# Optimization experiments

Measured on AMD Instinct MI355X. Metric: run time of the kernel, lower is better.

## Reference

```python
import jax, jax.numpy as jnp
import numpy as np
import math

D = 128
RATIO = 0.8
BN_EPS = 1e-5
N_NODES = 40000
N_EDGES = 640000
Y_SIZE = 8


def _prelu(x, a):
    return jnp.where(x > 0, x, a * x)


def setup_inputs() -> dict:
    key = jax.random.key(0)
    ks = jax.random.split(key, 16)
    inv = lambda n: 1.0 / np.sqrt(n)
    return {
        "x": jax.random.normal(ks[0], (N_NODES, 1), jnp.float32),
        "edge_index": jax.random.randint(ks[1], (2, N_EDGES), 0, N_NODES, jnp.int32),
        "W1": jax.random.normal(ks[2], (1, D), jnp.float32),
        "V1": jax.random.normal(ks[3], (1, D), jnp.float32),
        "Ws": jax.random.normal(ks[4], (9, D, D), jnp.float32) * inv(D),
        "Vs": jax.random.normal(ks[5], (9, D, D), jnp.float32) * inv(D),
        "conv_b": jax.random.normal(ks[6], (10, D), jnp.float32) * 0.01,
        "bn_gamma": 1.0 + 0.1 * jax.random.normal(ks[7], (10, D), jnp.float32),
        "bn_beta": 0.1 * jax.random.normal(ks[8], (10, D), jnp.float32),
        "bn_mean": jnp.zeros((10, D), jnp.float32),
        "bn_var": jnp.ones((10, D), jnp.float32),
        "pool_p": jax.random.normal(ks[9], (10, D), jnp.float32),
        "prelu_a": 0.25 * jnp.ones((1,), jnp.float32),
        "lin1_w": jax.random.normal(ks[10], (2560, 1280), jnp.float32) * inv(2560),
        "lin1_b": jax.random.normal(ks[11], (1280,), jnp.float32) * 0.01,
        "lin2_w": jax.random.normal(ks[12], (1280, Y_SIZE), jnp.float32) * inv(1280),
        "lin2_b": jax.random.normal(ks[13], (Y_SIZE,), jnp.float32) * 0.01,
    }


def reference(x, edge_index, W1, V1, Ws, Vs, conv_b, bn_gamma, bn_beta, bn_mean,
              bn_var, pool_p, prelu_a, lin1_w, lin1_b, lin2_w, lin2_b):
    # Single graph (batch all zeros). Edge array stays fixed size with a validity mask.
    src, dst = edge_index[0], edge_index[1]
    emask = jnp.ones(src.shape, dtype=bool)
    n = x.shape[0]
    h = x
    reads = []
    for i in range(10):
        W = W1 if i == 0 else Ws[i - 1]
        V = V1 if i == 0 else Vs[i - 1]
        # ---- ARMAConv (num_stacks=1, num_layers=1): relu(L_hat (h W) + h V + b)
        ew = emask.astype(h.dtype)
        deg = jax.ops.segment_sum(ew, dst, num_segments=n)
        dinv = jnp.where(deg > 0, 1.0 / jnp.sqrt(deg), 0.0)
        norm = dinv[dst] * dinv[src] * ew                      # [E]
        hw = h @ W                                             # [n, D]
        agg = jax.ops.segment_sum(hw[src] * norm[:, None], dst, num_segments=n)
        h = jax.nn.relu(agg + h @ V + conv_b[i])
        # ---- BatchNorm1d (eval mode, running stats)
        h = (h - bn_mean[i]) * (bn_gamma[i] / jnp.sqrt(bn_var[i] + BN_EPS)) + bn_beta[i]
        # ---- shared PReLU
        h = _prelu(h, prelu_a)
        # ---- TopKPooling(ratio=0.8): score = tanh(h.p/||p||), keep ceil(0.8n)
        p = pool_p[i]
        score = jnp.tanh(h @ p / jnp.linalg.norm(p))
        k = math.ceil(RATIO * n)
        topv, idx = jax.lax.top_k(score, k)
        h = h[idx] * topv[:, None]                             # [k, D]
        remap = jnp.full((n,), -1, jnp.int32).at[idx].set(jnp.arange(k, dtype=jnp.int32))
        ns, nd = remap[src], remap[dst]
        emask = emask & (ns >= 0) & (nd >= 0)
        src = jnp.where(emask, ns, 0)
        dst = jnp.where(emask, nd, 0)
        n = k
        # ---- global max + mean pool (single graph)
        reads.append(jnp.concatenate([h.max(axis=0), h.mean(axis=0)]))
    r = jnp.concatenate(reads)[None, :]                        # [1, 2560]
    z = _prelu(r @ lin1_w + lin1_b, prelu_a)                   # dropout = identity (eval)
    z = _prelu(z @ lin2_w + lin2_b, prelu_a)
    z = z - z.min(axis=1, keepdims=True)
    z = z / z.max(axis=1, keepdims=True)
    z = z / z.sum(axis=1, keepdims=True)
    return z
```

## Files before the change

kernel.cpp:

```cpp
#include <hip/hip_runtime.h>
#include <hip/hip_bf16.h>

#define NEDGE 640000
#define NMAX  40000
#define SB    40
#define PRB   256
#define EBLK  512
#define FB    1280
#define LIN1B 64
#define GRB   16
#define HTS   20
#define TKB   32
#define GHN   5632
#define GBMAX 2048

__device__ inline unsigned orderKey(float s) {
    unsigned b = __float_as_uint(s);
    return (b & 0x80000000u) ? ~b : (b | 0x80000000u);
}

__device__ inline void histAdd(int* sh, int bin, bool act, int nbits) {
    unsigned long long mm = __ballot(act);
    for (int b = 0; b < nbits; b++) {
        unsigned long long bal = __ballot(act && ((bin >> b) & 1));
        mm &= ((bin >> b) & 1) ? bal : ~bal;
    }
    if (act) {
        int lane = threadIdx.x & 63;
        int leader = __ffsll(mm) - 1;
        if (lane == leader) atomicAdd(&sh[bin], __popcll(mm));
    }
}

__device__ inline void gridbar(int* ctr, int target) {
    __syncthreads();
    if (threadIdx.x == 0) {
        __threadfence();
        __hip_atomic_fetch_add(ctr, 1, __ATOMIC_RELEASE, __HIP_MEMORY_SCOPE_AGENT);
        while (__hip_atomic_load(ctr, __ATOMIC_ACQUIRE, __HIP_MEMORY_SCOPE_AGENT) < target)
            __builtin_amdgcn_s_sleep(1);
        __threadfence();
    }
    __syncthreads();
}

__device__ inline int waveScanIncl(int v) {
    int lane = threadIdx.x & 63;
    #pragma unroll
    for (int off = 1; off < 64; off <<= 1) {
        int o = __shfl_up(v, off);
        if (lane >= off) v += o;
    }
    return v;
}

__device__ inline void selScan2048(const int* gh, int rem, int* outD, int* outR, int* outCnt) {
    __shared__ int wtot[16];
    __shared__ int s_T;
    int t = threadIdx.x, lane = t & 63, wid = t >> 6;
    int a0 = gh[2*t], a1 = gh[2*t+1];
    int s  = a0 + a1;
    int ws = waveScanIncl(s);
    if (lane == 63) wtot[wid] = ws;
    __syncthreads();
    if (t < 16) {
        int v = wtot[t];
        #pragma unroll
        for (int off = 1; off < 16; off <<= 1) { int o = __shfl_up(v, off); if (lane >= off) v += o; }
        wtot[t] = v;
        if (t == 15) s_T = v;
    }
    __syncthreads();
    int base = (wid > 0) ? wtot[wid-1] : 0;
    int inclPair = base + ws;
    int P1 = inclPair - a1;
    int P0 = P1 - a0;
    int Q = s_T - rem;
    if (a0 > 0 && P0 <= Q && Q < P0 + a0) { *outD = 2*t;   *outR = a0 - (Q - P0); *outCnt = a0; }
    if (a1 > 0 && P1 <= Q && Q < P1 + a1) { *outD = 2*t+1; *outR = a1 - (Q - P1); *outCnt = a1; }
    __syncthreads();
}

__device__ inline void selScan1024(const int* gh, int rem, int* outD, int* outR, int* outCnt) {
    __shared__ int wtot[16];
    __shared__ int s_T;
    int t = threadIdx.x, lane = t & 63, wid = t >> 6;
    int a0 = gh[t];
    int ws = waveScanIncl(a0);
    if (lane == 63) wtot[wid] = ws;
    __syncthreads();
    if (t < 16) {
        int v = wtot[t];
        #pragma unroll
        for (int off = 1; off < 16; off <<= 1) { int o = __shfl_up(v, off); if (lane >= off) v += o; }
        wtot[t] = v;
        if (t == 15) s_T = v;
    }
    __syncthreads();
    int base = (wid > 0) ? wtot[wid-1] : 0;
    int P0 = base + ws - a0;
    int Q = s_T - rem;
    if (a0 > 0 && P0 <= Q && Q < P0 + a0) { *outD = t; *outR = a0 - (Q - P0); *outCnt = a0; }
    __syncthreads();
}

__device__ inline void prefixSel256(int* lh, const int* gh, int rem, int* outD, int* outR) {
    int t = threadIdx.x;
    if (t < 256) lh[t] = gh[t];
    __syncthreads();
    for (int off = 1; off < 256; off <<= 1) {
        int v = 0;
        if (t < 256) v = lh[t] + ((t >= off) ? lh[t-off] : 0);
        __syncthreads();
        if (t < 256) lh[t] = v;
        __syncthreads();
    }
    if (t < 256) {
        int P = lh[t], Pp = (t == 0) ? 0 : lh[t-1];
        if (P >= rem && Pp < rem) { *outD = t; *outR = rem - Pp; }
    }
    __syncthreads();
}

__device__ inline void poolReduceC(const float* __restrict__ scr, float* __restrict__ rbuf,
                                   int gbP, int L, int ch) {
    int t = threadIdx.x;
    bool isMax = ch < 128;
    float acc = isMax ? -3.402823e38f : 0.f;
    for (int r = t; r < gbP; r += 256) {
        float v = scr[(size_t)r*256 + ch];
        acc = isMax ? fmaxf(acc, v) : (acc + v);
    }
    __shared__ float red[256];
    red[t] = acc; __syncthreads();
    for (int st = 128; st > 0; st >>= 1) {
        if (t < st) red[t] = isMax ? fmaxf(red[t], red[t+st]) : (red[t] + red[t+st]);
        __syncthreads();
    }
    if (t == 0) rbuf[L*256 + ch] = red[0];
}

__device__ const float c_invk[10] = {
    1.0f/32000.0f, 1.0f/25600.0f, 1.0f/20480.0f, 1.0f/16384.0f, 1.0f/13108.0f,
    1.0f/10487.0f, 1.0f/8390.0f,  1.0f/6712.0f,  1.0f/5370.0f,  1.0f/4296.0f };

__global__ void k_init(const int* __restrict__ eidx, int* __restrict__ esrc,
                       int* __restrict__ edst, int* __restrict__ erank,
                       const float* __restrict__ poolp,
                       float* __restrict__ rbuf, float* __restrict__ pnorm,
                       int* __restrict__ ecnt, int* __restrict__ degA,
                       int* __restrict__ tkc) {
    int b = blockIdx.x, t = threadIdx.x;
    if (b < 10) {
        rbuf[b*256 + t] = (t < 128) ? -3.402823e38f : 0.0f;
        __shared__ float red[256];
        float v = 0.0f;
        if (t < 128) { float pv = poolp[b*128 + t]; v = pv*pv; }
        red[t] = v; __syncthreads();
        for (int s = 128; s > 0; s >>= 1) { if (t < s) red[t] += red[t+s]; __syncthreads(); }
        if (t == 0) pnorm[b] = sqrtf(red[0]);
    }
    if (b == 10 && t < 16) ecnt[t] = (t == 0) ? NEDGE : 0;
    if (b == 11 && t < 64) tkc[t] = 0;
    int e = b*256 + t;
    if (e < NEDGE) {
        int d = eidx[NEDGE + e];
        esrc[e] = eidx[e]; edst[e] = d;
        erank[e] = atomicAdd(&degA[d], 1);
    }
}

__global__ __launch_bounds__(256) void k_presum(const int* __restrict__ deg,
                                                int* __restrict__ lbsum,
                                                int n, int chunk) {
    int b = blockIdx.x, t = threadIdx.x;
    __shared__ int red[256];
    int start = b*chunk, end = min(start + chunk, n);
    int s = 0;
    for (int i = start + t; i < end; i += 256) s += deg[i];
    red[t] = s; __syncthreads();
    for (int st = 128; st > 0; st >>= 1) { if (t < st) red[t] += red[t+st]; __syncthreads(); }
    if (t == 0) lbsum[b] = red[0];
}

__global__ void k_scan(const int* __restrict__ deg,
                       int* __restrict__ offs, float* __restrict__ dinv,
                       int* __restrict__ ghist, int* __restrict__ selbuf,
                       const int* __restrict__ lbsum,
                       const float* __restrict__ scr, float* __restrict__ rbuf,
                       int n, int chunk, int gbP, int prevL) {
    int b = blockIdx.x, t = threadIdx.x, lane = t & 63, wid = t >> 6;
    if (b >= SB) {
        if (gbP > 0) poolReduceC(scr, rbuf, gbP, prevL, b - SB);
        return;
    }
    __shared__ int s_excl;
    __shared__ int wsum[4];
    __shared__ int s_carry;
    __shared__ int s_sums[SB];
    if (b == 0) {
        for (int jj = t; jj < GHN; jj += 256) ghist[jj] = 0;
        if (t == 0) { selbuf[2] = 0; selbuf[5] = 0; }
    }
    if (t < SB) s_sums[t] = lbsum[t];
    __syncthreads();
    if (t == 0) {
        int excl = 0;
        for (int p = 0; p < b; p++) excl += s_sums[p];
        s_excl = excl;
    }
    __syncthreads();
    if (t == 0) s_carry = s_excl;
    __syncthreads();
    int start = b*chunk, end = min(start + chunk, n);
    for (int base = start; base < end; base += 256) {
        int i = base + t;
        int d = (i < end) ? deg[i] : 0;
        int incl = d;
        for (int off = 1; off < 64; off <<= 1) {
            int o = __shfl_up(incl, off);
            if (lane >= off) incl += o;
        }
        if (lane == 63) wsum[wid] = incl;
        __syncthreads();
        if (t == 0) { int c = s_carry; for (int w = 0; w < 4; w++) { int tmp = wsum[w]; wsum[w] = c; c += tmp; } s_carry = c; }
        __syncthreads();
        int p = wsum[wid] + incl - d;
        if (i < end) {
            offs[i] = p;
            dinv[i] = (d > 0) ? 1.0f/sqrtf((float)d) : 0.0f;
        }
        __syncthreads();
    }
}

__global__ __launch_bounds__(128) void k_fill(const int* __restrict__ esrc, const int* __restrict__ edst,
                                              const int* __restrict__ erank, const int* __restrict__ offs,
                                              int* __restrict__ csr, const int* __restrict__ ecnt) {
    int ec = *ecnt;
    for (int e = blockIdx.x*128 + threadIdx.x; e < ec; e += FB*128)
        csr[offs[edst[e]] + erank[e]] = esrc[e];
}

__global__ __launch_bounds__(128) void k_gather0(
    const float* __restrict__ x, const float* __restrict__ W1, const float* __restrict__ V1,
    const float* __restrict__ convb,
    const float* __restrict__ bng, const float* __restrict__ bnb,
    const float* __restrict__ bnm, const float* __restrict__ bnv,
    const float* __restrict__ poolp, const float* __restrict__ pnorm,
    const float* __restrict__ prelua,
    const int* __restrict__ offs, const int* __restrict__ deg, const float* __restrict__ dinv,
    const int* __restrict__ csr,
    float* __restrict__ AGG, float* __restrict__ score, unsigned* __restrict__ keys) {
    int v = blockIdx.x, j = threadIdx.x;
    __shared__ float red[128];
    int off = offs[v], dg = deg[v];
    float accs = 0.0f;
    for (int c = j; c < dg; c += 128) { int s = csr[off + c]; accs += x[s]*dinv[s]; }
    red[j] = accs; __syncthreads();
    for (int st = 64; st > 0; st >>= 1) { if (j < st) red[j] += red[j+st]; __syncthreads(); }
    float aggs = red[0] * dinv[v];
    __syncthreads();
    float h2 = aggs*W1[j] + x[v]*V1[j] + convb[j];
    h2 = fmaxf(h2, 0.0f);
    float scale = bng[j] / sqrtf(bnv[j] + 1e-5f);
    h2 = (h2 - bnm[j])*scale + bnb[j];
    float a = prelua[0];
    h2 = (h2 > 0.0f) ? h2 : a*h2;
    AGG[v*128 + j] = h2;
    red[j] = h2 * poolp[j]; __syncthreads();
    for (int st = 64; st > 0; st >>= 1) { if (j < st) red[j] += red[j+st]; __syncthreads(); }
    if (j == 0) {
        float sc = tanhf(red[0] / pnorm[0]);
        score[v] = sc;
        keys[v]  = orderKey(sc);
    }
}

__global__ __launch_bounds__(128) void k_gather(
    const float* __restrict__ HW, float* __restrict__ AGG,
    const int* __restrict__ offs, const int* __restrict__ deg, const float* __restrict__ dinv,
    const int* __restrict__ csr,
    const float* __restrict__ bng, const float* __restrict__ bnb,
    const float* __restrict__ bnm, const float* __restrict__ bnv,
    const float* __restrict__ poolp, const float* __restrict__ pnorm,
    const float* __restrict__ prelua,
    float* __restrict__ score, unsigned* __restrict__ keys, int layer) {
    int v = blockIdx.x, j = threadIdx.x;
    __shared__ int   s_src[128];
    __shared__ float s_dv[128];
    __shared__ float red[128];
    int off = offs[v], dg = deg[v];
    float acc = 0.0f;
    for (int base = 0; base < dg; base += 128) {
        int cnt = min(128, dg - base);
        if (j < cnt) { int s = csr[off + base + j]; s_src[j] = s; s_dv[j] = dinv[s]; }
        __syncthreads();
        for (int c = 0; c < cnt; c++) acc += HW[s_src[c]*128 + j] * s_dv[c];
        __syncthreads();
    }
    int gj = layer*128 + j;
    float h2 = AGG[v*128 + j] + acc*dinv[v];
    h2 = fmaxf(h2, 0.0f);
    float scale = bng[gj] / sqrtf(bnv[gj] + 1e-5f);
    h2 = (h2 - bnm[gj])*scale + bnb[gj];
    float a = prelua[0];
    h2 = (h2 > 0.0f) ? h2 : a*h2;
    AGG[v*128 + j] = h2;
    red[j] = h2 * poolp[gj]; __syncthreads();
    for (int st = 64; st > 0; st >>= 1) { if (j < st) red[j] += red[j+st]; __syncthreads(); }
    if (j == 0) {
        float sc = tanhf(red[0] / pnorm[layer]);
        score[v] = sc;
        keys[v]  = orderKey(sc);
    }
}

__global__ __launch_bounds__(1024) void k_topk(const unsigned* __restrict__ keys,
                                               int* __restrict__ gh, int* __restrict__ selbuf,
                                               int* __restrict__ degN,
                                               int* __restrict__ remap, int* __restrict__ keep_ids,
                                               int* __restrict__ bar, int n, int kk) {
    __shared__ int lh[2048];
    __shared__ int s_d1, s_r1, s_c1, s_dA, s_rA, s_cA, s_dB, s_ntk, s_cnt3, s_bC, s_r2, s_lowD, s_lowR;
    __shared__ int s_base, s_cur;
    int t = threadIdx.x, b = blockIdx.x, lane = t & 63;
    int* h1 = gh;
    int* h2 = gh + 2048;
    int* h3 = gh + 4096;
    int* h4 = gh + 5120;
    int* h5 = gh + 5376;

    for (int i = b*1024 + t; i < NMAX; i += TKB*1024) degN[i] = 0;

    int nR = (n + 1023) & ~1023;
    lh[t] = 0; lh[t+1024] = 0;
    __syncthreads();
    for (int i = b*1024 + t; i < nR; i += TKB*1024) {
        bool act = (i < n);
        int bin = act ? (int)(keys[i] >> 21) : 0;
        histAdd(lh, bin, act, 11);
    }
    __syncthreads();
    { int c = lh[t]; if (c) atomicAdd(&h1[t], c); c = lh[t+1024]; if (c) atomicAdd(&h1[t+1024], c); }
    gridbar(&bar[0], TKB);
    selScan2048(h1, kk, &s_d1, &s_r1, &s_c1);
    int bstar = s_d1;

    lh[t] = 0; lh[t+1024] = 0;
    __syncthreads();
    for (int i = b*1024 + t; i < nR; i += TKB*1024) {
        bool act = false; int bin = 0;
        if (i < n) { unsigned key = keys[i]; act = ((int)(key >> 21) == bstar); bin = (int)((key >> 10) & 2047); }
        histAdd(lh, act ? bin : 0, act, 11);
    }
    __syncthreads();
    { int c = lh[t]; if (c) atomicAdd(&h2[t], c); c = lh[t+1024]; if (c) atomicAdd(&h2[t+1024], c); }
    gridbar(&bar[1], TKB);
    selScan2048(h2, s_r1, &s_dA, &s_rA, &s_cA);
    unsigned top21 = ((unsigned)bstar << 11) | (unsigned)s_dA;

    lh[t] = 0;
    __syncthreads();
    for (int i = b*1024 + t; i < nR; i += TKB*1024) {
        bool act = false; int bin = 0;
        if (i < n) { unsigned key = keys[i]; act = ((key >> 10) == top21); bin = (int)(key & 1023); }
        histAdd(lh, act ? bin : 0, act, 10);
    }
    __syncthreads();
    { int c = lh[t]; if (c) atomicAdd(&h3[t], c); }
    gridbar(&bar[2], TKB);
    selScan1024(h3, s_rA, &s_dB, &s_ntk, &s_cnt3);
    unsigned thresh = (top21 << 10) | (unsigned)s_dB;

    int cut;
    if (s_cnt3 == s_ntk) {
        cut = n - 1;
    } else {
        if (t < 256) lh[t] = 0;
        __syncthreads();
        for (int i = b*1024 + t; i < n; i += TKB*1024)
            if (keys[i] == thresh) atomicAdd(&lh[i >> 8], 1);
        __syncthreads();
        if (t < 256) { int c = lh[t]; if (c) atomicAdd(&h4[t], c); }
        gridbar(&bar[3], TKB);
        prefixSel256(lh, h4, s_ntk, &s_bC, &s_r2);
        int bC = s_bC;

        if (t < 256) lh[t] = 0;
        __syncthreads();
        for (int i = b*1024 + t; i < n; i += TKB*1024)
            if (keys[i] == thresh && (i >> 8) == bC) atomicAdd(&lh[i & 255], 1);
        __syncthreads();
        if (t < 256) { int c = lh[t]; if (c) atomicAdd(&h5[t], c); }
        gridbar(&bar[4], TKB);
        prefixSel256(lh, h5, s_r2, &s_lowD, &s_lowR);
        cut = (bC << 8) | s_lowD;
    }

    {
        int cnt = 0;
        for (int base = b*1024; base < n; base += TKB*1024) {
            int i = base + t;
            if (i < n) {
                unsigned key = keys[i];
                cnt += (key > thresh) || (key == thresh && i <= cut);
            }
        }
        lh[t] = cnt; __syncthreads();
        for (int st = 512; st > 0; st >>= 1) { if (t < st) lh[t] += lh[t+st]; __syncthreads(); }
        if (t == 0) { s_base = atomicAdd(&selbuf[5], lh[0]); s_cur = 0; }
        __syncthreads();
        for (int base = b*1024; base < n; base += TKB*1024) {
            int i = base + t;
            bool keep = false;
            if (i < n) {
                unsigned key = keys[i];
                keep = (key > thresh) || (key == thresh && i <= cut);
            }
            unsigned long long m = __ballot(keep);
            int wcnt = __popcll(m);
            int wbase = 0;
            if (lane == 0 && wcnt) wbase = atomicAdd(&s_cur, wcnt);
            wbase = __shfl(wbase, 0);
            if (keep) {
                int slot = s_base + wbase + __popcll(m & ((1ULL << lane) - 1));
                remap[i] = slot; keep_ids[slot] = i;
            } else if (i < n) remap[i] = -1;
        }
    }
}

__global__ __launch_bounds__(128) void k_poolgemm(
        const float* __restrict__ AGGc, const float* __restrict__ score,
        const int* __restrict__ keep_ids, const int* __restrict__ remap,
        float* __restrict__ scr,
        const int* __restrict__ esrcP, const int* __restrict__ edstP,
        int* __restrict__ esrcN, int* __restrict__ edstN, int* __restrict__ erankN,
        const int* __restrict__ ecntP, int* __restrict__ ecntN, int* __restrict__ degN,
        const float* __restrict__ W, const float* __restrict__ V, const float* __restrict__ bias,
        float* __restrict__ HW, float* __restrict__ AGGn, int k, int gb, int do_gemm) {
    int b = blockIdx.x, t = threadIdx.x;
    __shared__ __align__(16) float ht[128*HTS];
    if (b < gb) {
        int v0 = b * GRB;
        float mx = -3.402823e38f, sm = 0.f;
        #pragma unroll
        for (int it = 0; it < GRB; it++) {
            int r = v0 + it;
            bool valid = (r < k);
            int vv = keep_ids[valid ? r : (k - 1)];
            float val = AGGc[(size_t)vv*128 + t] * score[vv];
            if (!valid) val = 0.f;
            ht[t*HTS + it] = val;
            if (valid) { mx = fmaxf(mx, val); sm += val; }
        }
        scr[b*256 + t]       = mx;
        scr[b*256 + 128 + t] = sm;
        if (!do_gemm) return;
        __syncthreads();
        float accW[GRB], accV[GRB];
        #pragma unroll
        for (int r = 0; r < GRB; r++) { accW[r] = 0.0f; accV[r] = 0.0f; }
        #pragma unroll 4
        for (int kk = 0; kk < 128; kk++) {
            float mw = W[kk*128 + t];
            float mv = V[kk*128 + t];
            const float* hp = &ht[kk*HTS];
            #pragma unroll
            for (int r4 = 0; r4 < GRB; r4 += 4) {
                float4 hq = *(const float4*)(hp + r4);
                accW[r4+0] += hq.x*mw;  accV[r4+0] += hq.x*mv;
                accW[r4+1] += hq.y*mw;  accV[r4+1] += hq.y*mv;
                accW[r4+2] += hq.z*mw;  accV[r4+2] += hq.z*mv;
                accW[r4+3] += hq.w*mw;  accV[r4+3] += hq.w*mv;
            }
        }
        float bb = bias[t];
        #pragma unroll
        for (int r = 0; r < GRB; r++) {
            int v = v0 + r;
            if (v >= k) break;
            HW[(size_t)v*128 + t]   = accW[r];
            AGGn[(size_t)v*128 + t] = accV[r] + bb;
        }
    } else {
        int eb = b - gb, lane = t & 63;
        int ec = *ecntP;
        int* red = (int*)ht;
        __shared__ int s_base, s_cur;
        int cnt = 0;
        for (int base = eb*128; base < ec; base += EBLK*128) {
            int e = base + t;
            if (e < ec) {
                int ns = remap[esrcP[e]], nd = remap[edstP[e]];
                cnt += (ns >= 0 && nd >= 0);
            }
        }
        red[t] = cnt; __syncthreads();
        for (int st = 64; st > 0; st >>= 1) { if (t < st) red[t] += red[t+st]; __syncthreads(); }
        if (t == 0) { s_base = atomicAdd(ecntN, red[0]); s_cur = 0; }
        __syncthreads();
        for (int base = eb*128; base < ec; base += EBLK*128) {
            int e = base + t;
            bool keep = false; int ns = 0, nd = 0;
            if (e < ec) {
                ns = remap[esrcP[e]]; nd = remap[edstP[e]];
                keep = (ns >= 0 && nd >= 0);
            }
            unsigned long long m = __ballot(keep);
            int wcnt = __popcll(m);
            int wbase = 0;
            if (lane == 0 && wcnt) wbase = atomicAdd(&s_cur, wcnt);
            wbase = __shfl(wbase, 0);
            if (keep) {
                int pos = s_base + wbase + __popcll(m & ((1ULL << lane) - 1));
                esrcN[pos] = ns; edstN[pos] = nd;
                erankN[pos] = atomicAdd(&degN[nd], 1);
            }
        }
    }
}

__global__ __launch_bounds__(256) void k_pred(const float* __restrict__ scr, float* __restrict__ rbuf,
                                              int gbP, int L) {
    poolReduceC(scr, rbuf, gbP, L, blockIdx.x);
}

__global__ __launch_bounds__(320) void k_lin1(const float* __restrict__ rbuf,
                                              const float* __restrict__ w1,
                                              float* __restrict__ z1part) {
    int b = blockIdx.x, t = threadIdx.x;
    int j = t*4;
    float4 acc = make_float4(0.f, 0.f, 0.f, 0.f);
    int i0 = b*40;
    for (int r = 0; r < 40; r++) {
        int i = i0 + r;
        float rv = rbuf[i];
        if (i & 128) rv *= c_invk[i >> 8];
        float4 w = *(const float4*)(w1 + (size_t)i*1280 + j);
        acc.x += rv*w.x; acc.y += rv*w.y; acc.z += rv*w.z; acc.w += rv*w.w;
    }
    *(float4*)(z1part + b*1280 + j) = acc;
}

__global__ __launch_bounds__(320) void k_lin2(const float* __restrict__ z1part,
                                              const float* __restrict__ b1,
                                              const float* __restrict__ w2, const float* __restrict__ b2,
                                              const float* __restrict__ prelua, float* __restrict__ out) {
    int t = threadIdx.x, lane = t & 63, wid = t >> 6;
    float a = prelua[0];
    int j = t*4;
    float4 acc = make_float4(0.f, 0.f, 0.f, 0.f);
    for (int p = 0; p < LIN1B; p++) {
        float4 v = *(const float4*)(z1part + p*1280 + j);
        acc.x += v.x; acc.y += v.y; acc.z += v.z; acc.w += v.w;
    }
    float4 bb = *(const float4*)(b1 + j);
    float z0 = acc.x + bb.x; z0 = z0 > 0.f ? z0 : a*z0;
    float z1 = acc.y + bb.y; z1 = z1 > 0.f ? z1 : a*z1;
    float z2 = acc.z + bb.z; z2 = z2 > 0.f ? z2 : a*z2;
    float z3 = acc.w + bb.w; z3 = z3 > 0.f ? z3 : a*z3;
    float s[8];
    #pragma unroll
    for (int o = 0; o < 8; o++)
        s[o] = z0*w2[(j+0)*8+o] + z1*w2[(j+1)*8+o] + z2*w2[(j+2)*8+o] + z3*w2[(j+3)*8+o];
    #pragma unroll
    for (int off = 32; off > 0; off >>= 1)
        #pragma unroll
        for (int o = 0; o < 8; o++) s[o] += __shfl_down(s[o], off);
    __shared__ float sred[5][8];
    if (lane == 0)
        for (int o = 0; o < 8; o++) sred[wid][o] = s[o];
    __syncthreads();
    if (t == 0) {
        float zo[8];
        for (int o = 0; o < 8; o++) {
            float z = sred[0][o]+sred[1][o]+sred[2][o]+sred[3][o]+sred[4][o] + b2[o];
            zo[o] = z > 0.f ? z : a*z;
        }
        float mn = zo[0];
        for (int o = 1; o < 8; o++) mn = fminf(mn, zo[o]);
        float v[8], mx = -3.402823e38f;
        for (int o = 0; o < 8; o++) { v[o] = zo[o] - mn; mx = fmaxf(mx, v[o]); }
        float sm = 0.f;
        for (int o = 0; o < 8; o++) { v[o] = v[o] / mx; sm += v[o]; }
        for (int o = 0; o < 8; o++) out[o] = v[o] / sm;
    }
}

extern "C" void kernel_launch(void* const* d_in, const int* in_sizes, int n_in,
                              void* d_out, int out_size, void* d_ws, size_t ws_size,
                              hipStream_t stream) {
    const float* x      = (const float*)d_in[0];
    const int*   eidx   = (const int*)  d_in[1];
    const float* W1     = (const float*)d_in[2];
    const float* V1     = (const float*)d_in[3];
    const float* Ws     = (const float*)d_in[4];
    const float* Vs     = (const float*)d_in[5];
    const float* convb  = (const float*)d_in[6];
    const float* bng    = (const float*)d_in[7];
    const float* bnb    = (const float*)d_in[8];
    const float* bnm    = (const float*)d_in[9];
    const float* bnv    = (const float*)d_in[10];
    const float* poolp  = (const float*)d_in[11];
    const float* prelua = (const float*)d_in[12];
    const float* w1     = (const float*)d_in[13];
    const float* b1     = (const float*)d_in[14];
    const float* w2     = (const float*)d_in[15];
    const float* b2     = (const float*)d_in[16];
    float* out = (float*)d_out;

    float* wsf  = (float*)d_ws;
    float* aggA   = wsf;
    float* aggB   = aggA  + (size_t)NMAX*128;
    float* HW     = aggB  + (size_t)NMAX*128;
    float* dinv   = HW    + (size_t)NMAX*128;
    float* score  = dinv  + NMAX;
    float* rbuf   = score + NMAX;
    float* pnorm  = rbuf  + 2560;
    float* z1part = pnorm + 16;
    float* scr    = z1part + LIN1B*1280;
    unsigned* keys = (unsigned*)(scr + (size_t)GBMAX*256);
    int* esrcA  = (int*)(keys + NMAX);
    int* edstA  = esrcA + NEDGE;
    int* erankA = edstA + NEDGE;
    int* esrcB  = erankA + NEDGE;
    int* edstB  = esrcB + NEDGE;
    int* erankB = edstB + NEDGE;
    int* csr    = erankB + NEDGE;
    int* degA   = csr   + NEDGE;
    int* degB   = degA  + NMAX;
    int* ghist  = degB  + NMAX;
    int* offs   = ghist + GHN;
    int* remap  = offs  + NMAX;
    int* keep_ids = remap + NMAX;
    int* lbsum  = keep_ids + NMAX;
    int* ecnt   = lbsum + SB*2;
    int* selbuf = ecnt  + 16;
    int* tkc    = selbuf + 16;

    static const int NS[10] = {40000,32000,25600,20480,16384,13108,10487,8390,6712,5370};
    static const int KS[10] = {32000,25600,20480,16384,13108,10487,8390,6712,5370,4296};

    hipMemsetAsync(degA, 0, (size_t)NMAX*sizeof(int), stream);
    k_init<<<2500, 256, 0, stream>>>(eidx, esrcA, edstA, erankA, poolp, rbuf, pnorm,
                                     ecnt, degA, tkc);

    for (int i = 0; i < 10; i++) {
        int n = NS[i], k = KS[i];
        int chunk = (n + SB - 1) / SB;
        int* esrcP  = (i & 1) ? esrcB  : esrcA;
        int* edstP  = (i & 1) ? edstB  : edstA;
        int* erankP = (i & 1) ? erankB : erankA;
        int* esrcN  = (i & 1) ? esrcA  : esrcB;
        int* edstN  = (i & 1) ? edstA  : edstB;
        int* erankN = (i & 1) ? erankA : erankB;
        int* degP   = (i & 1) ? degB : degA;
        int* degN   = (i & 1) ? degA : degB;
        float* AGGc = (i & 1) ? aggB : aggA;
        float* AGGn = (i & 1) ? aggA : aggB;

        int gbP = (i == 0) ? 0 : (KS[i-1] + GRB - 1) / GRB;
        k_presum<<<SB, 256, 0, stream>>>(degP, lbsum, n, chunk);
        k_scan<<<SB + PRB, 256, 0, stream>>>(degP, offs, dinv, ghist, selbuf,
                                             lbsum, scr, rbuf, n, chunk,
                                             gbP, i - 1);

        k_fill<<<FB, 128, 0, stream>>>(esrcP, edstP, erankP, offs, csr, &ecnt[i]);

        if (i == 0) {
            k_gather0<<<n, 128, 0, stream>>>(x, W1, V1, convb,
                                             bng, bnb, bnm, bnv, poolp, pnorm, prelua,
                                             offs, degP, dinv, csr, AGGc, score, keys);
        } else {
            k_gather<<<n, 128, 0, stream>>>(HW, AGGc, offs, degP, dinv, csr,
                                            bng, bnb, bnm, bnv, poolp, pnorm, prelua,
                                            score, keys, i);
        }

        k_topk<<<TKB, 1024, 0, stream>>>(keys, ghist, selbuf, degN,
                                         remap, keep_ids, tkc + i*5, n, k);

        int gb = (k + GRB - 1) / GRB;
        int do_gemm = (i < 9);
        int grid = gb + (do_gemm ? EBLK : 0);
        k_poolgemm<<<grid, 128, 0, stream>>>(AGGc, score, keep_ids, remap, scr,
                                             esrcP, edstP, esrcN, edstN, erankN,
                                             &ecnt[i], &ecnt[i+1], degN,
                                             Ws + (size_t)min(i,8)*16384,
                                             Vs + (size_t)min(i,8)*16384,
                                             convb + min(i+1,9)*128,
                                             HW, AGGn, k, gb, do_gemm);
    }

    k_pred<<<PRB, 256, 0, stream>>>(scr, rbuf, (KS[9] + GRB - 1) / GRB, 9);
    k_lin1<<<LIN1B, 320, 0, stream>>>(rbuf, w1, z1part);
    k_lin2<<<1, 320, 0, stream>>>(z1part, b1, w2, b2, prelua, out);
}
```

Measured before the change: 978.7 us.

## Fuse block-sum pass into scan via grid barrier, move degN clear, unroll gather

```diff
diff --git a/kernel.cpp b/kernel.cpp
--- a/kernel.cpp
+++ b/kernel.cpp
@@ -10,9 +10,9 @@
 #define LIN1B 64
 #define GRB   16
 #define HTS   20
-#define TKB   32
+#define TKB   64
 #define GHN   5632
-#define GBMAX 2048
+#define GBMAX 4096
 
 __device__ inline unsigned orderKey(float s) {
     unsigned b = __float_as_uint(s);
@@ -149,7 +149,7 @@
                        const float* __restrict__ poolp,
                        float* __restrict__ rbuf, float* __restrict__ pnorm,
                        int* __restrict__ ecnt, int* __restrict__ degA,
-                       int* __restrict__ tkc) {
+                       int* __restrict__ tkc, int* __restrict__ sbar) {
     int b = blockIdx.x, t = threadIdx.x;
     if (b < 10) {
         rbuf[b*256 + t] = (t < 128) ? -3.402823e38f : 0.0f;
@@ -161,7 +161,10 @@
         if (t == 0) pnorm[b] = sqrtf(red[0]);
     }
     if (b == 10 && t < 16) ecnt[t] = (t == 0) ? NEDGE : 0;
-    if (b == 11 && t < 64) tkc[t] = 0;
+    if (b == 11) {
+        if (t < 64) tkc[t] = 0;
+        else if (t == 64) sbar[0] = 0;
+    }
     int e = b*256 + t;
     if (e < NEDGE) {
         int d = eidx[NEDGE + e];
@@ -170,30 +173,19 @@
     }
 }
 
-__global__ __launch_bounds__(256) void k_presum(const int* __restrict__ deg,
-                                                int* __restrict__ lbsum,
-                                                int n, int chunk) {
-    int b = blockIdx.x, t = threadIdx.x;
-    __shared__ int red[256];
-    int start = b*chunk, end = min(start + chunk, n);
-    int s = 0;
-    for (int i = start + t; i < end; i += 256) s += deg[i];
-    red[t] = s; __syncthreads();
-    for (int st = 128; st > 0; st >>= 1) { if (t < st) red[t] += red[t+st]; __syncthreads(); }
-    if (t == 0) lbsum[b] = red[0];
-}
-
 __global__ void k_scan(const int* __restrict__ deg,
                        int* __restrict__ offs, float* __restrict__ dinv,
                        int* __restrict__ ghist, int* __restrict__ selbuf,
-                       const int* __restrict__ lbsum,
+                       int* __restrict__ lbsum, int* __restrict__ sbar,
+                       int* __restrict__ degN,
                        const float* __restrict__ scr, float* __restrict__ rbuf,
-                       int n, int chunk, int gbP, int prevL) {
+                       int n, int chunk, int epoch, int gbP, int prevL) {
     int b = blockIdx.x, t = threadIdx.x, lane = t & 63, wid = t >> 6;
     if (b >= SB) {
         if (gbP > 0) poolReduceC(scr, rbuf, gbP, prevL, b - SB);
         return;
     }
+    __shared__ int red[256];
     __shared__ int s_excl;
     __shared__ int wsum[4];
     __shared__ int s_carry;
@@ -202,7 +194,22 @@
         for (int jj = t; jj < GHN; jj += 256) ghist[jj] = 0;
         if (t == 0) { selbuf[2] = 0; selbuf[5] = 0; }
     }
-    if (t < SB) s_sums[t] = lbsum[t];
+    for (int i = b*256 + t; i < NMAX; i += SB*256) degN[i] = 0;
+    int start = b*chunk, end = min(start + chunk, n);
+    int s = 0;
+    for (int i = start + t; i < end; i += 256) s += deg[i];
+    red[t] = s; __syncthreads();
+    for (int st = 128; st > 0; st >>= 1) { if (t < st) red[t] += red[t+st]; __syncthreads(); }
+    if (t == 0) {
+        __hip_atomic_store(&lbsum[b], red[0], __ATOMIC_RELAXED, __HIP_MEMORY_SCOPE_AGENT);
+        __threadfence();
+        __hip_atomic_fetch_add(&sbar[0], 1, __ATOMIC_RELEASE, __HIP_MEMORY_SCOPE_AGENT);
+        while (__hip_atomic_load(&sbar[0], __ATOMIC_ACQUIRE, __HIP_MEMORY_SCOPE_AGENT) < epoch*SB)
+            __builtin_amdgcn_s_sleep(1);
+        __threadfence();
+    }
+    __syncthreads();
+    if (t < SB) s_sums[t] = __hip_atomic_load(&lbsum[t], __ATOMIC_RELAXED, __HIP_MEMORY_SCOPE_AGENT);
     __syncthreads();
     if (t == 0) {
         int excl = 0;
@@ -212,7 +219,6 @@
     __syncthreads();
     if (t == 0) s_carry = s_excl;
     __syncthreads();
-    int start = b*chunk, end = min(start + chunk, n);
     for (int base = start; base < end; base += 256) {
         int i = base + t;
         int d = (i < end) ? deg[i] : 0;
@@ -296,7 +302,17 @@
         int cnt = min(128, dg - base);
         if (j < cnt) { int s = csr[off + base + j]; s_src[j] = s; s_dv[j] = dinv[s]; }
         __syncthreads();
-        for (int c = 0; c < cnt; c++) acc += HW[s_src[c]*128 + j] * s_dv[c];
+        int c = 0;
+        for (; c + 4 <= cnt; c += 4) {
+            int s0 = s_src[c], s1 = s_src[c+1], s2 = s_src[c+2], s3 = s_src[c+3];
+            float d0 = s_dv[c], d1 = s_dv[c+1], d2 = s_dv[c+2], d3 = s_dv[c+3];
+            float h0 = HW[(size_t)s0*128 + j];
+            float h1 = HW[(size_t)s1*128 + j];
+            float h2 = HW[(size_t)s2*128 + j];
+            float h3 = HW[(size_t)s3*128 + j];
+            acc += h0*d0; acc += h1*d1; acc += h2*d2; acc += h3*d3;
+        }
+        for (; c < cnt; c++) acc += HW[(size_t)s_src[c]*128 + j] * s_dv[c];
         __syncthreads();
     }
     int gj = layer*128 + j;
@@ -318,7 +334,6 @@
 
 __global__ __launch_bounds__(1024) void k_topk(const unsigned* __restrict__ keys,
                                                int* __restrict__ gh, int* __restrict__ selbuf,
-                                               int* __restrict__ degN,
                                                int* __restrict__ remap, int* __restrict__ keep_ids,
                                                int* __restrict__ bar, int n, int kk) {
     __shared__ int lh[2048];
@@ -330,8 +345,6 @@
     int* h3 = gh + 4096;
     int* h4 = gh + 5120;
     int* h5 = gh + 5376;
-
-    for (int i = b*1024 + t; i < NMAX; i += TKB*1024) degN[i] = 0;
 
     int nR = (n + 1023) & ~1023;
     lh[t] = 0; lh[t+1024] = 0;
@@ -636,7 +649,8 @@
     int* remap  = offs  + NMAX;
     int* keep_ids = remap + NMAX;
     int* lbsum  = keep_ids + NMAX;
-    int* ecnt   = lbsum + SB*2;
+    int* sbar   = lbsum + SB*2;
+    int* ecnt   = sbar + SB;
     int* selbuf = ecnt  + 16;
     int* tkc    = selbuf + 16;
 
@@ -645,7 +659,7 @@
 
     hipMemsetAsync(degA, 0, (size_t)NMAX*sizeof(int), stream);
     k_init<<<2500, 256, 0, stream>>>(eidx, esrcA, edstA, erankA, poolp, rbuf, pnorm,
-                                     ecnt, degA, tkc);
+                                     ecnt, degA, tkc, sbar);
 
     for (int i = 0; i < 10; i++) {
         int n = NS[i], k = KS[i];
@@ -662,10 +676,9 @@
         float* AGGn = (i & 1) ? aggA : aggB;
 
         int gbP = (i == 0) ? 0 : (KS[i-1] + GRB - 1) / GRB;
-        k_presum<<<SB, 256, 0, stream>>>(degP, lbsum, n, chunk);
         k_scan<<<SB + PRB, 256, 0, stream>>>(degP, offs, dinv, ghist, selbuf,
-                                             lbsum, scr, rbuf, n, chunk,
-                                             gbP, i - 1);
+                                             lbsum, sbar, degN, scr, rbuf, n, chunk,
+                                             i + 1, gbP, i - 1);
 
         k_fill<<<FB, 128, 0, stream>>>(esrcP, edstP, erankP, offs, csr, &ecnt[i]);
 
@@ -679,7 +692,7 @@
                                             score, keys, i);
         }
 
-        k_topk<<<TKB, 1024, 0, stream>>>(keys, ghist, selbuf, degN,
+        k_topk<<<TKB, 1024, 0, stream>>>(keys, ghist, selbuf,
                                          remap, keep_ids, tkc + i*5, n, k);
 
         int gb = (k + GRB - 1) / GRB;
```

New measurement: 1.048 ms. +7.1%, slower.

## Fuse first top-k histogram into gather, move degN clearing, widen topk grid

Applied to the files above, without the earlier changes.

```diff
diff --git a/kernel.cpp b/kernel.cpp
--- a/kernel.cpp
+++ b/kernel.cpp
@@ -10,9 +10,9 @@
 #define LIN1B 64
 #define GRB   16
 #define HTS   20
-#define TKB   32
+#define TKB   64
 #define GHN   5632
-#define GBMAX 2048
+#define GBMAX 4096
 
 __device__ inline unsigned orderKey(float s) {
     unsigned b = __float_as_uint(s);
@@ -172,9 +172,11 @@
 
 __global__ __launch_bounds__(256) void k_presum(const int* __restrict__ deg,
                                                 int* __restrict__ lbsum,
+                                                int* __restrict__ degN,
                                                 int n, int chunk) {
     int b = blockIdx.x, t = threadIdx.x;
     __shared__ int red[256];
+    for (int i = b*256 + t; i < NMAX; i += SB*256) degN[i] = 0;
     int start = b*chunk, end = min(start + chunk, n);
     int s = 0;
     for (int i = start + t; i < end; i += 256) s += deg[i];
@@ -251,7 +253,8 @@
     const float* __restrict__ prelua,
     const int* __restrict__ offs, const int* __restrict__ deg, const float* __restrict__ dinv,
     const int* __restrict__ csr,
-    float* __restrict__ AGG, float* __restrict__ score, unsigned* __restrict__ keys) {
+    float* __restrict__ AGG, float* __restrict__ score, unsigned* __restrict__ keys,
+    int* __restrict__ h1) {
     int v = blockIdx.x, j = threadIdx.x;
     __shared__ float red[128];
     int off = offs[v], dg = deg[v];
@@ -273,7 +276,9 @@
     if (j == 0) {
         float sc = tanhf(red[0] / pnorm[0]);
         score[v] = sc;
-        keys[v]  = orderKey(sc);
+        unsigned key = orderKey(sc);
+        keys[v] = key;
+        atomicAdd(&h1[key >> 21], 1);
     }
 }
 
@@ -285,7 +290,8 @@
     const float* __restrict__ bnm, const float* __restrict__ bnv,
     const float* __restrict__ poolp, const float* __restrict__ pnorm,
     const float* __restrict__ prelua,
-    float* __restrict__ score, unsigned* __restrict__ keys, int layer) {
+    float* __restrict__ score, unsigned* __restrict__ keys, int layer,
+    int* __restrict__ h1) {
     int v = blockIdx.x, j = threadIdx.x;
     __shared__ int   s_src[128];
     __shared__ float s_dv[128];
@@ -296,7 +302,17 @@
         int cnt = min(128, dg - base);
         if (j < cnt) { int s = csr[off + base + j]; s_src[j] = s; s_dv[j] = dinv[s]; }
         __syncthreads();
-        for (int c = 0; c < cnt; c++) acc += HW[s_src[c]*128 + j] * s_dv[c];
+        int c = 0;
+        for (; c + 4 <= cnt; c += 4) {
+            int s0 = s_src[c], s1 = s_src[c+1], s2 = s_src[c+2], s3 = s_src[c+3];
+            float d0 = s_dv[c], d1 = s_dv[c+1], d2 = s_dv[c+2], d3 = s_dv[c+3];
+            float h0 = HW[(size_t)s0*128 + j];
+            float h1v = HW[(size_t)s1*128 + j];
+            float h2v = HW[(size_t)s2*128 + j];
+            float h3 = HW[(size_t)s3*128 + j];
+            acc += h0*d0; acc += h1v*d1; acc += h2v*d2; acc += h3*d3;
+        }
+        for (; c < cnt; c++) acc += HW[(size_t)s_src[c]*128 + j] * s_dv[c];
         __syncthreads();
     }
     int gj = layer*128 + j;
@@ -312,13 +328,14 @@
     if (j == 0) {
         float sc = tanhf(red[0] / pnorm[layer]);
         score[v] = sc;
-        keys[v]  = orderKey(sc);
+        unsigned key = orderKey(sc);
+        keys[v] = key;
+        atomicAdd(&h1[key >> 21], 1);
     }
 }
 
 __global__ __launch_bounds__(1024) void k_topk(const unsigned* __restrict__ keys,
                                                int* __restrict__ gh, int* __restrict__ selbuf,
-                                               int* __restrict__ degN,
                                                int* __restrict__ remap, int* __restrict__ keep_ids,
                                                int* __restrict__ bar, int n, int kk) {
     __shared__ int lh[2048];
@@ -331,19 +348,7 @@
     int* h4 = gh + 5120;
     int* h5 = gh + 5376;
 
-    for (int i = b*1024 + t; i < NMAX; i += TKB*1024) degN[i] = 0;
-
     int nR = (n + 1023) & ~1023;
-    lh[t] = 0; lh[t+1024] = 0;
-    __syncthreads();
-    for (int i = b*1024 + t; i < nR; i += TKB*1024) {
-        bool act = (i < n);
-        int bin = act ? (int)(keys[i] >> 21) : 0;
-        histAdd(lh, bin, act, 11);
-    }
-    __syncthreads();
-    { int c = lh[t]; if (c) atomicAdd(&h1[t], c); c = lh[t+1024]; if (c) atomicAdd(&h1[t+1024], c); }
-    gridbar(&bar[0], TKB);
     selScan2048(h1, kk, &s_d1, &s_r1, &s_c1);
     int bstar = s_d1;
 
@@ -662,7 +667,7 @@
         float* AGGn = (i & 1) ? aggA : aggB;
 
         int gbP = (i == 0) ? 0 : (KS[i-1] + GRB - 1) / GRB;
-        k_presum<<<SB, 256, 0, stream>>>(degP, lbsum, n, chunk);
+        k_presum<<<SB, 256, 0, stream>>>(degP, lbsum, degN, n, chunk);
         k_scan<<<SB + PRB, 256, 0, stream>>>(degP, offs, dinv, ghist, selbuf,
                                              lbsum, scr, rbuf, n, chunk,
                                              gbP, i - 1);
@@ -672,14 +677,14 @@
         if (i == 0) {
             k_gather0<<<n, 128, 0, stream>>>(x, W1, V1, convb,
                                              bng, bnb, bnm, bnv, poolp, pnorm, prelua,
-                                             offs, degP, dinv, csr, AGGc, score, keys);
+                                             offs, degP, dinv, csr, AGGc, score, keys, ghist);
         } else {
             k_gather<<<n, 128, 0, stream>>>(HW, AGGc, offs, degP, dinv, csr,
                                             bng, bnb, bnm, bnv, poolp, pnorm, prelua,
-                                            score, keys, i);
-        }
-
-        k_topk<<<TKB, 1024, 0, stream>>>(keys, ghist, selbuf, degN,
+                                            score, keys, i, ghist);
+        }
+
+        k_topk<<<TKB, 1024, 0, stream>>>(keys, ghist, selbuf,
                                          remap, keep_ids, tkc + i*5, n, k);
 
         int gb = (k + GRB - 1) / GRB;
```

Measured after the change: 2.376 ms. +142.8%, slower.
